# Performance work log

Hardware: AMD Instinct MI355X
Metric: run time of the kernel (lower is better)

## Reference

```python
import jax, jax.numpy as jnp
import numpy as np

N = 50000        # nodes
E_RAND = 800000  # random edges (avg degree 16)
F_IN = 512       # num_features
H = 128          # h_dim * num_heads = 16 * 8
C = 40           # num_classes
NEG_SLOPE = 0.2  # GATv2 default


def _glorot(key, shape):
    lim = float(np.sqrt(6.0 / (shape[0] + shape[1])))
    return jax.random.uniform(key, shape, jnp.float32, -lim, lim)


def setup_inputs() -> dict:
    key = jax.random.key(0)
    ks = jax.random.split(key, 12)
    src = jax.random.randint(ks[0], (E_RAND,), 0, N)
    dst = jax.random.randint(ks[1], (E_RAND,), 0, N)
    loop = jnp.arange(N)  # self-loops (GATv2Conv add_self_loops=True)
    edge_index = jnp.stack([jnp.concatenate([src, loop]),
                            jnp.concatenate([dst, loop])]).astype(jnp.int32)
    x = jax.random.normal(ks[2], (N, F_IN), jnp.float32)
    return {
        "x": x,
        "edge_index": edge_index,
        "W1l": _glorot(ks[3], (F_IN, H)), "b1l": jnp.zeros((H,), jnp.float32),
        "W1r": _glorot(ks[4], (F_IN, H)), "b1r": jnp.zeros((H,), jnp.float32),
        "a1": _glorot(ks[5], (H, 1)).reshape(H),
        "bias1": jnp.zeros((H,), jnp.float32),
        "W2l": _glorot(ks[6], (H, C)), "b2l": jnp.zeros((C,), jnp.float32),
        "W2r": _glorot(ks[7], (H, C)), "b2r": jnp.zeros((C,), jnp.float32),
        "a2": _glorot(ks[8], (C, 1)).reshape(C),
        "bias2": jnp.zeros((C,), jnp.float32),
    }


def gatv2_layer(x, src, dst, Wl, bl, Wr, br, att, bias, n):
    # PyG GATv2Conv, heads=1: xl = lin_l(x) (source side), xr = lin_r(x) (target side)
    xl = x @ Wl + bl                                   # [N, C_out]
    xr = x @ Wr + br                                   # [N, C_out]
    # edge score e_ij = a^T LeakyReLU(xl[j] + xr[i])
    e = jax.nn.leaky_relu(xl[src] + xr[dst], negative_slope=NEG_SLOPE) @ att  # [E]
    # segment softmax over edges grouped by destination node
    m = jax.ops.segment_max(e, dst, num_segments=n)    # every node has a self-loop
    ex = jnp.exp(e - m[dst])
    den = jax.ops.segment_sum(ex, dst, num_segments=n)
    alpha = ex / den[dst]                              # [E]
    # weighted scatter-aggregate of source-transformed features
    out = jax.ops.segment_sum(alpha[:, None] * xl[src], dst, num_segments=n)
    return out + bias


def reference(x, edge_index, W1l, b1l, W1r, b1r, a1, bias1,
              W2l, b2l, W2r, b2r, a2, bias2):
    # eval mode: dropout(p=0.6) is identity
    src, dst = edge_index[0], edge_index[1]
    n = x.shape[0]
    h = gatv2_layer(x, src, dst, W1l, b1l, W1r, b1r, a1, bias1, n)
    h = jax.nn.elu(h)
    h = gatv2_layer(h, src, dst, W2l, b2l, W2r, b2r, a2, bias2, n)
    return (h, jax.nn.log_softmax(h, axis=1))
```

## Files before the change

kernel.cpp:

```cpp
#include <hip/hip_runtime.h>
#include <hip/hip_bf16.h>
#include <math.h>

#define FIN 512
#define H1 128
#define C2 40
#define C2P 64

typedef __attribute__((ext_vector_type(8))) short short8;
typedef __attribute__((ext_vector_type(4))) float f32x4;

__device__ __forceinline__ ushort f2bf(float f) {
    union { float f; unsigned u; } c; c.f = f;
    unsigned u = c.u;
    return (ushort)((u + 0x7fffu + ((u >> 16) & 1u)) >> 16);
}
__device__ __forceinline__ float bf2f_lo(unsigned u) { return __uint_as_float(u << 16); }
__device__ __forceinline__ float bf2f_hi(unsigned u) { return __uint_as_float(u & 0xffff0000u); }

__device__ __forceinline__ short bfc(float f) {
    __hip_bfloat16 h = __float2bfloat16(f);
    return *reinterpret_cast<short*>(&h);
}

__device__ __forceinline__ void gload_lds16(const void* g, void* l) {
    __builtin_amdgcn_global_load_lds(
        (const __attribute__((address_space(1))) void*)g,
        (__attribute__((address_space(3))) void*)l, 16, 0, 0);
}

__global__ void count_k(const int* __restrict__ dst, int* __restrict__ cnt, int E) {
    int e = blockIdx.x * 256 + threadIdx.x;
    if (e < E) atomicAdd(&cnt[dst[e] + 1], 1);
}

__global__ __launch_bounds__(1024) void scan_k(int* __restrict__ arr, int ntot) {
    __shared__ int part[1024];
    int t = threadIdx.x;
    int chunk = (((ntot + 1023) / 1024) + 3) & ~3;
    int b = t * chunk;
    int s = 0;
    bool full = (b + chunk <= ntot);
    if (full) {
#pragma unroll 4
        for (int j = 0; j < chunk; j += 4) {
            int4 v = *reinterpret_cast<const int4*>(&arr[b + j]);
            s += v.x + v.y + v.z + v.w;
        }
    } else {
        for (int j = b; j < ntot; j++) s += arr[j];
    }
    part[t] = s;
    __syncthreads();
    for (int off = 1; off < 1024; off <<= 1) {
        int v = (t >= off) ? part[t - off] : 0;
        __syncthreads();
        part[t] += v;
        __syncthreads();
    }
    int run = (t == 0) ? 0 : part[t - 1];
    if (full) {
        for (int j = 0; j < chunk; j += 4) {
            int4 v = *reinterpret_cast<const int4*>(&arr[b + j]);
            int r0 = run + v.x, r1 = r0 + v.y, r2 = r1 + v.z, r3 = r2 + v.w;
            *reinterpret_cast<int4*>(&arr[b + j]) = make_int4(r0, r1, r2, r3);
            run = r3;
        }
    } else {
        for (int j = b; j < ntot; j++) { run += arr[j]; arr[j] = run; }
    }
}

__global__ void fill_k(const int* __restrict__ src, const int* __restrict__ dst,
                       const int* __restrict__ rowptr, int* __restrict__ fillp,
                       int* __restrict__ csr, int E) {
    int e = blockIdx.x * 256 + threadIdx.x;
    if (e < E) {
        int d = dst[e];
        int p = atomicAdd(&fillp[d], 1);
        csr[rowptr[d] + p] = src[e];
    }
}

__global__ void prep_k(const float* __restrict__ W1l, const float* __restrict__ W1r,
                       ushort* __restrict__ Wt2) {
    int idx = blockIdx.x * 256 + threadIdx.x;
    int kc  = idx >> 11;
    int rem = idx & 2047;
    int col = rem >> 3;
    int j   = rem & 7;
    int k   = kc * 8 + j;
    float v = (col < H1) ? W1l[k * H1 + col] : W1r[k * H1 + (col - H1)];
    Wt2[idx] = f2bf(v);
}

__global__ void prep2_k(const float* __restrict__ W2l, const float* __restrict__ W2r,
                        ushort* __restrict__ Ws) {
    int idx = blockIdx.x * 256 + threadIdx.x;
    if (idx >= 80 * H1) return;
    int col = idx >> 7;
    int k   = idx & 127;
    float v = (col < C2) ? W2l[k * C2 + col] : W2r[k * C2 + (col - C2)];
    Ws[idx] = f2bf(v);
}

__global__ __launch_bounds__(256, 3) void gemm1_k(
    const float* __restrict__ x, const ushort* __restrict__ Wt2,
    const float* __restrict__ bl, const float* __restrict__ br,
    ushort* __restrict__ xlb, float* __restrict__ xr, int n)
{
    __shared__ ushort As[2][64][40];
    __shared__ ushort Bs[2][4 * 256 * 8];

    const int tid  = threadIdx.x;
    const int w    = tid >> 6;
    const int lane = tid & 63;
    const int l15  = lane & 15;
    const int lhi  = lane >> 4;
    const int r0   = blockIdx.x * 64;

    f32x4 acc[4][4];
#pragma unroll
    for (int m = 0; m < 4; m++)
#pragma unroll
        for (int nn = 0; nn < 4; nn++) acc[m][nn] = (f32x4){0.f, 0.f, 0.f, 0.f};

    const int arow = tid >> 2;
    const int akq  = (tid & 3) * 8;
    const int arow_g = min(r0 + arow, n - 1);
    const float* aptr = x + (size_t)arow_g * FIN + akq;

    const char* bsrc = (const char*)Wt2 + (size_t)tid * 16;
    char*       bdst = (char*)Bs + (size_t)tid * 16;

    {
        float4 v0 = *reinterpret_cast<const float4*>(aptr);
        float4 v1 = *reinterpret_cast<const float4*>(aptr + 4);
#pragma unroll
        for (int i = 0; i < 4; i++)
            gload_lds16(bsrc + i * 4096, bdst + i * 4096);
        short8 h0;
        h0[0] = bfc(v0.x); h0[1] = bfc(v0.y); h0[2] = bfc(v0.z); h0[3] = bfc(v0.w);
        h0[4] = bfc(v1.x); h0[5] = bfc(v1.y); h0[6] = bfc(v1.z); h0[7] = bfc(v1.w);
        *reinterpret_cast<short8*>(&As[0][arow][akq]) = h0;
    }
    __syncthreads();

    int cur = 0;
    for (int t = 0; t < 15; ++t) {
        const int nxt = cur ^ 1;

        float4 v0 = *reinterpret_cast<const float4*>(aptr + (t + 1) * 32);
        float4 v1 = *reinterpret_cast<const float4*>(aptr + (t + 1) * 32 + 4);
        {
            const char* bs = bsrc + (size_t)(t + 1) * 16384;
            char*       bd = bdst + (size_t)nxt * 16384;
#pragma unroll
            for (int i = 0; i < 4; i++)
                gload_lds16(bs + i * 4096, bd + i * 4096);
        }

        short8 af[4], bf4[4];
#pragma unroll
        for (int m = 0; m < 4; m++)
            af[m] = *reinterpret_cast<const short8*>(&As[cur][m * 16 + l15][lhi * 8]);
#pragma unroll
        for (int nn = 0; nn < 4; nn++)
            bf4[nn] = *reinterpret_cast<const short8*>(
                &Bs[cur][(lhi * 256 + w * 64 + nn * 16 + l15) * 8]);
#pragma unroll
        for (int m = 0; m < 4; m++)
#pragma unroll
            for (int nn = 0; nn < 4; nn++)
                acc[m][nn] = __builtin_amdgcn_mfma_f32_16x16x32_bf16(af[m], bf4[nn], acc[m][nn], 0, 0, 0);

        short8 h0;
        h0[0] = bfc(v0.x); h0[1] = bfc(v0.y); h0[2] = bfc(v0.z); h0[3] = bfc(v0.w);
        h0[4] = bfc(v1.x); h0[5] = bfc(v1.y); h0[6] = bfc(v1.z); h0[7] = bfc(v1.w);
        *reinterpret_cast<short8*>(&As[nxt][arow][akq]) = h0;

        __syncthreads();
        cur = nxt;
    }

    {
        short8 af[4], bf4[4];
#pragma unroll
        for (int m = 0; m < 4; m++)
            af[m] = *reinterpret_cast<const short8*>(&As[cur][m * 16 + l15][lhi * 8]);
#pragma unroll
        for (int nn = 0; nn < 4; nn++)
            bf4[nn] = *reinterpret_cast<const short8*>(
                &Bs[cur][(lhi * 256 + w * 64 + nn * 16 + l15) * 8]);
#pragma unroll
        for (int m = 0; m < 4; m++)
#pragma unroll
            for (int nn = 0; nn < 4; nn++)
                acc[m][nn] = __builtin_amdgcn_mfma_f32_16x16x32_bf16(af[m], bf4[nn], acc[m][nn], 0, 0, 0);
    }

#pragma unroll
    for (int nn = 0; nn < 4; nn++) {
        int col = w * 64 + nn * 16 + l15;
        bool left = (col < H1);
        float bias = left ? bl[col] : br[col - H1];
#pragma unroll
        for (int m = 0; m < 4; m++) {
#pragma unroll
            for (int r = 0; r < 4; r++) {
                int row = r0 + m * 16 + lhi * 4 + r;
                if (row < n) {
                    float v = acc[m][nn][r] + bias;
                    if (left) xlb[(size_t)row * H1 + col] = f2bf(v);
                    else      xr [(size_t)row * H1 + (col - H1)] = v;
                }
            }
        }
    }
}

__global__ __launch_bounds__(256) void edge1_k(
    const ushort* __restrict__ xlb, const float* xr,
    const int* __restrict__ rowptr, const int* __restrict__ csr,
    const float* __restrict__ att, const float* __restrict__ bias,
    float* h, int n)
{
    int wid  = threadIdx.x >> 6;
    int lane = threadIdx.x & 63;
    int grp  = lane >> 4;
    int gl   = lane & 15;
    int i = blockIdx.x * 4 + wid;
    if (i >= n) return;

    const float* xrp = &xr[(size_t)i * H1 + gl * 8];
    float4 xr0 = *reinterpret_cast<const float4*>(xrp);
    float4 xr1v = *reinterpret_cast<const float4*>(xrp + 4);
    float xrv[8] = {xr0.x, xr0.y, xr0.z, xr0.w, xr1v.x, xr1v.y, xr1v.z, xr1v.w};
    float4 a0 = *reinterpret_cast<const float4*>(&att[gl * 8]);
    float4 a1 = *reinterpret_cast<const float4*>(&att[gl * 8 + 4]);
    float av[8] = {a0.x, a0.y, a0.z, a0.w, a1.x, a1.y, a1.z, a1.w};

    int e0 = rowptr[i], e1 = rowptr[i + 1];

    float m = -INFINITY, den = 0.f;
    float acc[8];
#pragma unroll
    for (int f = 0; f < 8; f++) acc[f] = 0.f;

    int e = e0 + grp;
    uint4 u0, u1;
    if (e < e1) {
        int s = csr[e];
        u0 = *reinterpret_cast<const uint4*>(&xlb[(size_t)s * H1 + gl * 8]);
    }
    if (e + 4 < e1) {
        int s = csr[e + 4];
        u1 = *reinterpret_cast<const uint4*>(&xlb[(size_t)s * H1 + gl * 8]);
    }
    while (e < e1) {
        uint4 cu = u0;
        u0 = u1;
        if (e + 8 < e1) {
            int s2 = csr[e + 8];
            u1 = *reinterpret_cast<const uint4*>(&xlb[(size_t)s2 * H1 + gl * 8]);
        }
        float xlv[8];
        xlv[0] = bf2f_lo(cu.x); xlv[1] = bf2f_hi(cu.x);
        xlv[2] = bf2f_lo(cu.y); xlv[3] = bf2f_hi(cu.y);
        xlv[4] = bf2f_lo(cu.z); xlv[5] = bf2f_hi(cu.z);
        xlv[6] = bf2f_lo(cu.w); xlv[7] = bf2f_hi(cu.w);
        float p = 0.f;
#pragma unroll
        for (int f = 0; f < 8; f++) {
            float t = xlv[f] + xrv[f];
            t = t > 0.f ? t : 0.2f * t;
            p += t * av[f];
        }
#pragma unroll
        for (int o = 8; o > 0; o >>= 1) p += __shfl_xor(p, o);
        float mn = fmaxf(m, p);
        float sc = __expf(m - mn);
        float wgt = __expf(p - mn);
        den = den * sc + wgt;
#pragma unroll
        for (int f = 0; f < 8; f++) acc[f] = acc[f] * sc + wgt * xlv[f];
        m = mn;
        e += 4;
    }

    float mstar = m;
    mstar = fmaxf(mstar, __shfl_xor(mstar, 16));
    mstar = fmaxf(mstar, __shfl_xor(mstar, 32));
    float scale = __expf(m - mstar);
    den *= scale;
#pragma unroll
    for (int f = 0; f < 8; f++) acc[f] *= scale;
    den += __shfl_xor(den, 16); den += __shfl_xor(den, 32);
#pragma unroll
    for (int f = 0; f < 8; f++) {
        acc[f] += __shfl_xor(acc[f], 16);
        acc[f] += __shfl_xor(acc[f], 32);
    }

    if (grp == 0) {
        float inv = 1.f / den;
        float o[8];
#pragma unroll
        for (int f = 0; f < 8; f++) {
            float v = acc[f] * inv + bias[gl * 8 + f];
            o[f] = v > 0.f ? v : expm1f(v);
        }
        float* hp = &h[(size_t)i * H1 + gl * 8];
        *reinterpret_cast<float4*>(hp)     = make_float4(o[0], o[1], o[2], o[3]);
        *reinterpret_cast<float4*>(hp + 4) = make_float4(o[4], o[5], o[6], o[7]);
    }
}

__global__ __launch_bounds__(256) void gemm2_k(
    const float* __restrict__ h, const ushort* __restrict__ Ws,
    const float* __restrict__ bl, const float* __restrict__ br,
    ushort* __restrict__ xl2b, float* __restrict__ xr2, int n)
{
    __shared__ ushort WsL[80][136];

    const int tid = threadIdx.x;
    const int w    = tid >> 6;
    const int lane = tid & 63;
    const int l15  = lane & 15;
    const int lhi  = lane >> 4;
    const int r0 = blockIdx.x * 64;

#pragma unroll
    for (int q = 0; q < 5; q++) {
        int c = tid + q * 256;
        int col = c >> 4;
        int k0  = (c & 15) * 8;
        *reinterpret_cast<short8*>(&WsL[col][k0]) =
            *reinterpret_cast<const short8*>(&Ws[col * H1 + k0]);
    }
    __syncthreads();

    const int arow = min(r0 + w * 16 + l15, n - 1);
    const float* ap = &h[(size_t)arow * H1 + lhi * 8];

    f32x4 acc[5];
#pragma unroll
    for (int nt = 0; nt < 5; nt++) acc[nt] = (f32x4){0.f, 0.f, 0.f, 0.f};

#pragma unroll
    for (int kc = 0; kc < 4; kc++) {
        float4 v0 = *reinterpret_cast<const float4*>(ap + kc * 32);
        float4 v1 = *reinterpret_cast<const float4*>(ap + kc * 32 + 4);
        short8 af;
        af[0] = bfc(v0.x); af[1] = bfc(v0.y);
        af[2] = bfc(v0.z); af[3] = bfc(v0.w);
        af[4] = bfc(v1.x); af[5] = bfc(v1.y);
        af[6] = bfc(v1.z); af[7] = bfc(v1.w);
#pragma unroll
        for (int nt = 0; nt < 5; nt++) {
            short8 bf = *reinterpret_cast<const short8*>(&WsL[nt * 16 + l15][kc * 32 + lhi * 8]);
            acc[nt] = __builtin_amdgcn_mfma_f32_16x16x32_bf16(af, bf, acc[nt], 0, 0, 0);
        }
    }

#pragma unroll
    for (int nt = 0; nt < 5; nt++) {
        int col = nt * 16 + l15;
        float bias = (col < C2) ? bl[col] : br[col - C2];
#pragma unroll
        for (int r = 0; r < 4; r++) {
            int row = r0 + w * 16 + lhi * 4 + r;
            if (row < n) {
                float v = acc[nt][r] + bias;
                if (col < C2) xl2b[(size_t)row * C2P + col] = f2bf(v);
                else          xr2 [(size_t)row * C2  + (col - C2)] = v;
            }
        }
    }
    {
        int row = r0 + w * 16 + l15;
        int part = lhi;
        if (part < 3 && row < n) {
            uint4 z = make_uint4(0u, 0u, 0u, 0u);
            *reinterpret_cast<uint4*>(&xl2b[(size_t)row * C2P + C2 + part * 8]) = z;
        }
    }
}

__global__ __launch_bounds__(256) void edge2_k(
    const ushort* __restrict__ xl2b, const float* __restrict__ xr2,
    const int* __restrict__ rowptr, const int* __restrict__ csr,
    const float* __restrict__ att, const float* __restrict__ bias,
    float* __restrict__ out, int n)
{
    int wid  = threadIdx.x >> 6;
    int lane = threadIdx.x & 63;
    int grp  = lane >> 3;
    int gl   = lane & 7;
    int i = blockIdx.x * 4 + wid;
    if (i >= n) return;

    float xrv[8], av[8];
#pragma unroll
    for (int f = 0; f < 8; f++) {
        int idx = gl * 8 + f;
        bool real = idx < C2;
        xrv[f] = real ? xr2[(size_t)i * C2 + idx] : 0.f;
        av[f]  = real ? att[idx] : 0.f;
    }

    int e0 = rowptr[i], e1 = rowptr[i + 1];

    float m = -INFINITY, den = 0.f;
    float acc[8];
#pragma unroll
    for (int f = 0; f < 8; f++) acc[f] = 0.f;

    int e = e0 + grp;
    uint4 u0, u1;
    if (e < e1) {
        int s = csr[e];
        u0 = *reinterpret_cast<const uint4*>(&xl2b[(size_t)s * C2P + gl * 8]);
    }
    if (e + 8 < e1) {
        int s = csr[e + 8];
        u1 = *reinterpret_cast<const uint4*>(&xl2b[(size_t)s * C2P + gl * 8]);
    }
    while (e < e1) {
        uint4 cu = u0;
        u0 = u1;
        if (e + 16 < e1) {
            int s2 = csr[e + 16];
            u1 = *reinterpret_cast<const uint4*>(&xl2b[(size_t)s2 * C2P + gl * 8]);
        }
        float xlv[8];
        xlv[0] = bf2f_lo(cu.x); xlv[1] = bf2f_hi(cu.x);
        xlv[2] = bf2f_lo(cu.y); xlv[3] = bf2f_hi(cu.y);
        xlv[4] = bf2f_lo(cu.z); xlv[5] = bf2f_hi(cu.z);
        xlv[6] = bf2f_lo(cu.w); xlv[7] = bf2f_hi(cu.w);
        float p = 0.f;
#pragma unroll
        for (int f = 0; f < 8; f++) {
            float t = xlv[f] + xrv[f];
            t = t > 0.f ? t : 0.2f * t;
            p += t * av[f];
        }
#pragma unroll
        for (int o = 4; o > 0; o >>= 1) p += __shfl_xor(p, o);
        float mn = fmaxf(m, p);
        float sc = __expf(m - mn);
        float wgt = __expf(p - mn);
        den = den * sc + wgt;
#pragma unroll
        for (int f = 0; f < 8; f++) acc[f] = acc[f] * sc + wgt * xlv[f];
        m = mn;
        e += 8;
    }

    float mstar = m;
    mstar = fmaxf(mstar, __shfl_xor(mstar, 8));
    mstar = fmaxf(mstar, __shfl_xor(mstar, 16));
    mstar = fmaxf(mstar, __shfl_xor(mstar, 32));
    float scale = __expf(m - mstar);
    den *= scale;
#pragma unroll
    for (int f = 0; f < 8; f++) acc[f] *= scale;
    den += __shfl_xor(den, 8); den += __shfl_xor(den, 16); den += __shfl_xor(den, 32);
#pragma unroll
    for (int f = 0; f < 8; f++) {
        acc[f] += __shfl_xor(acc[f], 8);
        acc[f] += __shfl_xor(acc[f], 16);
        acc[f] += __shfl_xor(acc[f], 32);
    }

    float inv = 1.f / den;
    bool real_lane = gl < 5;
    float o[8];
#pragma unroll
    for (int f = 0; f < 8; f++) {
        int idx = gl * 8 + f;
        o[f] = acc[f] * inv + (idx < C2 ? bias[idx] : 0.f);
    }

    float mv = -INFINITY;
    if (real_lane) {
#pragma unroll
        for (int f = 0; f < 8; f++) mv = fmaxf(mv, o[f]);
    }
    mv = fmaxf(mv, __shfl_xor(mv, 1));
    mv = fmaxf(mv, __shfl_xor(mv, 2));
    mv = fmaxf(mv, __shfl_xor(mv, 4));
    float se = 0.f;
    if (real_lane) {
#pragma unroll
        for (int f = 0; f < 8; f++) se += __expf(o[f] - mv);
    }
    se += __shfl_xor(se, 1); se += __shfl_xor(se, 2); se += __shfl_xor(se, 4);
    float lse = mv + logf(se);

    if (grp == 0 && real_lane) {
        float* op = &out[(size_t)i * C2 + gl * 8];
        *reinterpret_cast<float4*>(op)     = make_float4(o[0], o[1], o[2], o[3]);
        *reinterpret_cast<float4*>(op + 4) = make_float4(o[4], o[5], o[6], o[7]);
        float* lp = &out[(size_t)n * C2 + (size_t)i * C2 + gl * 8];
        *reinterpret_cast<float4*>(lp)     = make_float4(o[0] - lse, o[1] - lse, o[2] - lse, o[3] - lse);
        *reinterpret_cast<float4*>(lp + 4) = make_float4(o[4] - lse, o[5] - lse, o[6] - lse, o[7] - lse);
    }
}

extern "C" void kernel_launch(void* const* d_in, const int* in_sizes, int n_in,
                              void* d_out, int out_size, void* d_ws, size_t ws_size,
                              hipStream_t stream) {
    const float* x    = (const float*)d_in[0];
    const int*   ei   = (const int*)  d_in[1];
    const float* W1l  = (const float*)d_in[2];
    const float* b1l  = (const float*)d_in[3];
    const float* W1r  = (const float*)d_in[4];
    const float* b1r  = (const float*)d_in[5];
    const float* a1   = (const float*)d_in[6];
    const float* bias1= (const float*)d_in[7];
    const float* W2l  = (const float*)d_in[8];
    const float* b2l  = (const float*)d_in[9];
    const float* W2r  = (const float*)d_in[10];
    const float* b2r  = (const float*)d_in[11];
    const float* a2   = (const float*)d_in[12];
    const float* bias2= (const float*)d_in[13];

    const int N = in_sizes[0] / FIN;
    const int E = in_sizes[1] / 2;
    const int* src = ei;
    const int* dst = ei + E;

    float*  xr1 = (float*)d_ws;
    float*  xr2 = xr1 + (size_t)N * H1;
    ushort* xlb = (ushort*)(xr2 + (size_t)N * C2);
    ushort* xl2b = xlb;
    ushort* Wt2 = xlb + (size_t)N * H1;
    ushort* Ws2 = Wt2 + 131072;
    int* rowptr = (int*)(Ws2 + 10240);
    int* fillp  = rowptr + (N + 1);
    int* csr    = fillp + N;

    hipMemsetAsync(rowptr, 0, sizeof(int) * (size_t)(2 * N + 1), stream);
    count_k<<<(E + 255) / 256, 256, 0, stream>>>(dst, rowptr, E);
    scan_k<<<1, 1024, 0, stream>>>(rowptr, N + 1);
    fill_k<<<(E + 255) / 256, 256, 0, stream>>>(src, dst, rowptr, fillp, csr, E);

    prep_k<<<512, 256, 0, stream>>>(W1l, W1r, Wt2);
    prep2_k<<<40, 256, 0, stream>>>(W2l, W2r, Ws2);
    gemm1_k<<<(N + 63) / 64, 256, 0, stream>>>(x, Wt2, b1l, b1r, xlb, xr1, N);
    edge1_k<<<(N + 3) / 4, 256, 0, stream>>>(xlb, xr1, rowptr, csr, a1, bias1, xr1, N);
    gemm2_k<<<(N + 63) / 64, 256, 0, stream>>>(xr1, Ws2, b2l, b2r, xl2b, xr2, N);
    edge2_k<<<(N + 3) / 4, 256, 0, stream>>>(xl2b, xr2, rowptr, csr, a2, bias2, (float*)d_out, N);
}
```

Measured before the change: 306.3 us.

## Split gemm1 output columns across two blocks and merge prep kernels into count

Merges the edge-count, W1 prep and W2 prep kernels into one launch to cut launch overhead. Splits gemm1 so each block computes either the xl or the xr half (128 columns), doubling the grid, halving the B tile and accumulator registers, and raising the occupancy hint to 6. The trade-off is that every x tile is now read and converted to bf16 twice, once per half, in exchange for more parallelism and occupancy.

```diff
diff --git a/kernel.cpp b/kernel.cpp
--- a/kernel.cpp
+++ b/kernel.cpp
@@ -29,9 +29,34 @@
         (__attribute__((address_space(3))) void*)l, 16, 0, 0);
 }
 
-__global__ void count_k(const int* __restrict__ dst, int* __restrict__ cnt, int E) {
-    int e = blockIdx.x * 256 + threadIdx.x;
-    if (e < E) atomicAdd(&cnt[dst[e] + 1], 1);
+__global__ void aux_k(const int* __restrict__ dst, int* __restrict__ cnt, int E, int EB,
+                      const float* __restrict__ W1l, const float* __restrict__ W1r,
+                      ushort* __restrict__ Wt2,
+                      const float* __restrict__ W2l, const float* __restrict__ W2r,
+                      ushort* __restrict__ Ws) {
+    int b = blockIdx.x;
+    int t = threadIdx.x;
+    if (b < EB) {
+        int e = b * 256 + t;
+        if (e < E) atomicAdd(&cnt[dst[e] + 1], 1);
+    } else if (b < EB + 512) {
+        int idx = (b - EB) * 256 + t;
+        int kc  = idx >> 11;
+        int rem = idx & 2047;
+        int col = rem >> 3;
+        int j   = rem & 7;
+        int k   = kc * 8 + j;
+        float v = (col < H1) ? W1l[k * H1 + col] : W1r[k * H1 + (col - H1)];
+        Wt2[idx] = f2bf(v);
+    } else {
+        int idx = (b - EB - 512) * 256 + t;
+        if (idx < 80 * H1) {
+            int col = idx >> 7;
+            int k   = idx & 127;
+            float v = (col < C2) ? W2l[k * C2 + col] : W2r[k * C2 + (col - C2)];
+            Ws[idx] = f2bf(v);
+        }
+    }
 }
 
 __global__ __launch_bounds__(1024) void scan_k(int* __restrict__ arr, int ntot) {
@@ -82,63 +107,44 @@
     }
 }
 
-__global__ void prep_k(const float* __restrict__ W1l, const float* __restrict__ W1r,
-                       ushort* __restrict__ Wt2) {
-    int idx = blockIdx.x * 256 + threadIdx.x;
-    int kc  = idx >> 11;
-    int rem = idx & 2047;
-    int col = rem >> 3;
-    int j   = rem & 7;
-    int k   = kc * 8 + j;
-    float v = (col < H1) ? W1l[k * H1 + col] : W1r[k * H1 + (col - H1)];
-    Wt2[idx] = f2bf(v);
-}
-
-__global__ void prep2_k(const float* __restrict__ W2l, const float* __restrict__ W2r,
-                        ushort* __restrict__ Ws) {
-    int idx = blockIdx.x * 256 + threadIdx.x;
-    if (idx >= 80 * H1) return;
-    int col = idx >> 7;
-    int k   = idx & 127;
-    float v = (col < C2) ? W2l[k * C2 + col] : W2r[k * C2 + (col - C2)];
-    Ws[idx] = f2bf(v);
-}
-
-__global__ __launch_bounds__(256, 3) void gemm1_k(
+__global__ __launch_bounds__(256, 6) void gemm1_k(
     const float* __restrict__ x, const ushort* __restrict__ Wt2,
     const float* __restrict__ bl, const float* __restrict__ br,
     ushort* __restrict__ xlb, float* __restrict__ xr, int n)
 {
     __shared__ ushort As[2][64][40];
-    __shared__ ushort Bs[2][4 * 256 * 8];
+    __shared__ ushort Bs[2][4 * 128 * 8];
 
     const int tid  = threadIdx.x;
     const int w    = tid >> 6;
     const int lane = tid & 63;
     const int l15  = lane & 15;
     const int lhi  = lane >> 4;
-    const int r0   = blockIdx.x * 64;
-
-    f32x4 acc[4][4];
+    const int bm   = blockIdx.x >> 1;
+    const int half = blockIdx.x & 1;
+    const int r0   = bm * 64;
+    const int c0   = half * 128;
+
+    f32x4 acc[4][2];
 #pragma unroll
     for (int m = 0; m < 4; m++)
 #pragma unroll
-        for (int nn = 0; nn < 4; nn++) acc[m][nn] = (f32x4){0.f, 0.f, 0.f, 0.f};
+        for (int nn = 0; nn < 2; nn++) acc[m][nn] = (f32x4){0.f, 0.f, 0.f, 0.f};
 
     const int arow = tid >> 2;
     const int akq  = (tid & 3) * 8;
     const int arow_g = min(r0 + arow, n - 1);
     const float* aptr = x + (size_t)arow_g * FIN + akq;
 
-    const char* bsrc = (const char*)Wt2 + (size_t)tid * 16;
-    char*       bdst = (char*)Bs + (size_t)tid * 16;
+    const char* bsrc = (const char*)Wt2 + ((size_t)w * 256 + c0) * 16 + (size_t)lane * 16;
+    char*       bdst = (char*)Bs + (size_t)w * 2048 + (size_t)lane * 16;
 
     {
+#pragma unroll
+        for (int h2 = 0; h2 < 2; h2++)
+            gload_lds16(bsrc + h2 * 1024, bdst + h2 * 1024);
         float4 v0 = *reinterpret_cast<const float4*>(aptr);
         float4 v1 = *reinterpret_cast<const float4*>(aptr + 4);
-#pragma unroll
-        for (int i = 0; i < 4; i++)
-            gload_lds16(bsrc + i * 4096, bdst + i * 4096);
         short8 h0;
         h0[0] = bfc(v0.x); h0[1] = bfc(v0.y); h0[2] = bfc(v0.z); h0[3] = bfc(v0.w);
         h0[4] = bfc(v1.x); h0[5] = bfc(v1.y); h0[6] = bfc(v1.z); h0[7] = bfc(v1.w);
@@ -154,25 +160,25 @@
         float4 v1 = *reinterpret_cast<const float4*>(aptr + (t + 1) * 32 + 4);
         {
             const char* bs = bsrc + (size_t)(t + 1) * 16384;
-            char*       bd = bdst + (size_t)nxt * 16384;
-#pragma unroll
-            for (int i = 0; i < 4; i++)
-                gload_lds16(bs + i * 4096, bd + i * 4096);
-        }
-
-        short8 af[4], bf4[4];
+            char*       bd = bdst + (size_t)nxt * 8192;
+#pragma unroll
+            for (int h2 = 0; h2 < 2; h2++)
+                gload_lds16(bs + h2 * 1024, bd + h2 * 1024);
+        }
+
+        short8 af[4], bf2[2];
 #pragma unroll
         for (int m = 0; m < 4; m++)
             af[m] = *reinterpret_cast<const short8*>(&As[cur][m * 16 + l15][lhi * 8]);
 #pragma unroll
-        for (int nn = 0; nn < 4; nn++)
-            bf4[nn] = *reinterpret_cast<const short8*>(
-                &Bs[cur][(lhi * 256 + w * 64 + nn * 16 + l15) * 8]);
+        for (int nn = 0; nn < 2; nn++)
+            bf2[nn] = *reinterpret_cast<const short8*>(
+                &Bs[cur][(lhi * 128 + w * 32 + nn * 16 + l15) * 8]);
 #pragma unroll
         for (int m = 0; m < 4; m++)
 #pragma unroll
-            for (int nn = 0; nn < 4; nn++)
-                acc[m][nn] = __builtin_amdgcn_mfma_f32_16x16x32_bf16(af[m], bf4[nn], acc[m][nn], 0, 0, 0);
+            for (int nn = 0; nn < 2; nn++)
+                acc[m][nn] = __builtin_amdgcn_mfma_f32_16x16x32_bf16(af[m], bf2[nn], acc[m][nn], 0, 0, 0);
 
         short8 h0;
         h0[0] = bfc(v0.x); h0[1] = bfc(v0.y); h0[2] = bfc(v0.z); h0[3] = bfc(v0.w);
@@ -184,26 +190,25 @@
     }
 
     {
-        short8 af[4], bf4[4];
+        short8 af[4], bf2[2];
 #pragma unroll
         for (int m = 0; m < 4; m++)
             af[m] = *reinterpret_cast<const short8*>(&As[cur][m * 16 + l15][lhi * 8]);
 #pragma unroll
-        for (int nn = 0; nn < 4; nn++)
-            bf4[nn] = *reinterpret_cast<const short8*>(
-                &Bs[cur][(lhi * 256 + w * 64 + nn * 16 + l15) * 8]);
+        for (int nn = 0; nn < 2; nn++)
+            bf2[nn] = *reinterpret_cast<const short8*>(
+                &Bs[cur][(lhi * 128 + w * 32 + nn * 16 + l15) * 8]);
 #pragma unroll
         for (int m = 0; m < 4; m++)
 #pragma unroll
-            for (int nn = 0; nn < 4; nn++)
-                acc[m][nn] = __builtin_amdgcn_mfma_f32_16x16x32_bf16(af[m], bf4[nn], acc[m][nn], 0, 0, 0);
-    }
-
-#pragma unroll
-    for (int nn = 0; nn < 4; nn++) {
-        int col = w * 64 + nn * 16 + l15;
-        bool left = (col < H1);
-        float bias = left ? bl[col] : br[col - H1];
+            for (int nn = 0; nn < 2; nn++)
+                acc[m][nn] = __builtin_amdgcn_mfma_f32_16x16x32_bf16(af[m], bf2[nn], acc[m][nn], 0, 0, 0);
+    }
+
+#pragma unroll
+    for (int nn = 0; nn < 2; nn++) {
+        int col = w * 32 + nn * 16 + l15;
+        float bias = half ? br[col] : bl[col];
 #pragma unroll
         for (int m = 0; m < 4; m++) {
 #pragma unroll
@@ -211,8 +216,8 @@
                 int row = r0 + m * 16 + lhi * 4 + r;
                 if (row < n) {
                     float v = acc[m][nn][r] + bias;
-                    if (left) xlb[(size_t)row * H1 + col] = f2bf(v);
-                    else      xr [(size_t)row * H1 + (col - H1)] = v;
+                    if (half) xr [(size_t)row * H1 + col] = v;
+                    else      xlb[(size_t)row * H1 + col] = f2bf(v);
                 }
             }
         }
@@ -541,14 +546,14 @@
     int* fillp  = rowptr + (N + 1);
     int* csr    = fillp + N;
 
+    const int EB = (E + 255) / 256;
+
     hipMemsetAsync(rowptr, 0, sizeof(int) * (size_t)(2 * N + 1), stream);
-    count_k<<<(E + 255) / 256, 256, 0, stream>>>(dst, rowptr, E);
+    aux_k<<<EB + 552, 256, 0, stream>>>(dst, rowptr, E, EB, W1l, W1r, Wt2, W2l, W2r, Ws2);
     scan_k<<<1, 1024, 0, stream>>>(rowptr, N + 1);
-    fill_k<<<(E + 255) / 256, 256, 0, stream>>>(src, dst, rowptr, fillp, csr, E);
-
-    prep_k<<<512, 256, 0, stream>>>(W1l, W1r, Wt2);
-    prep2_k<<<40, 256, 0, stream>>>(W2l, W2r, Ws2);
-    gemm1_k<<<(N + 63) / 64, 256, 0, stream>>>(x, Wt2, b1l, b1r, xlb, xr1, N);
+    fill_k<<<EB, 256, 0, stream>>>(src, dst, rowptr, fillp, csr, E);
+
+    gemm1_k<<<((N + 63) / 64) * 2, 256, 0, stream>>>(x, Wt2, b1l, b1r, xlb, xr1, N);
     edge1_k<<<(N + 3) / 4, 256, 0, stream>>>(xlb, xr1, rowptr, csr, a1, bias1, xr1, N);
     gemm2_k<<<(N + 63) / 64, 256, 0, stream>>>(xr1, Ws2, b2l, b2r, xl2b, xr2, N);
     edge2_k<<<(N + 3) / 4, 256, 0, stream>>>(xl2b, xr2, rowptr, csr, a2, bias2, (float*)d_out, N);
```

New measurement: 302.1 us. Within noise of the previous version (-1.4%).

## Stage full A tile in LDS, stream B from global via registers; merge prep kernels

Applied to the files above, without the earlier changes.

The first GEMM now loads the entire 64x512 row block of x into LDS as bf16 once, instead of double-buffering 32-wide K slices with a barrier per step. B fragments are read directly from global (L2-resident weights) into registers, with two register sets alternating as a prefetch. Occupancy drops from 3 to 2 blocks per CU because the LDS tile is larger. Separately, the edge-count, W1 and W2 prep kernels are fused into one launch to cut launch overhead.

```diff
diff --git a/kernel.cpp b/kernel.cpp
--- a/kernel.cpp
+++ b/kernel.cpp
@@ -23,15 +23,34 @@
     return *reinterpret_cast<short*>(&h);
 }
 
-__device__ __forceinline__ void gload_lds16(const void* g, void* l) {
-    __builtin_amdgcn_global_load_lds(
-        (const __attribute__((address_space(1))) void*)g,
-        (__attribute__((address_space(3))) void*)l, 16, 0, 0);
-}
-
-__global__ void count_k(const int* __restrict__ dst, int* __restrict__ cnt, int E) {
-    int e = blockIdx.x * 256 + threadIdx.x;
-    if (e < E) atomicAdd(&cnt[dst[e] + 1], 1);
+__global__ void aux_k(const int* __restrict__ dst, int* __restrict__ cnt, int E, int EB,
+                      const float* __restrict__ W1l, const float* __restrict__ W1r,
+                      ushort* __restrict__ Wt2,
+                      const float* __restrict__ W2l, const float* __restrict__ W2r,
+                      ushort* __restrict__ Ws) {
+    int b = blockIdx.x;
+    int t = threadIdx.x;
+    if (b < EB) {
+        int e = b * 256 + t;
+        if (e < E) atomicAdd(&cnt[dst[e] + 1], 1);
+    } else if (b < EB + 512) {
+        int idx = (b - EB) * 256 + t;
+        int kc  = idx >> 11;
+        int rem = idx & 2047;
+        int col = rem >> 3;
+        int j   = rem & 7;
+        int k   = kc * 8 + j;
+        float v = (col < H1) ? W1l[k * H1 + col] : W1r[k * H1 + (col - H1)];
+        Wt2[idx] = f2bf(v);
+    } else {
+        int idx = (b - EB - 512) * 256 + t;
+        if (idx < 80 * H1) {
+            int col = idx >> 7;
+            int k   = idx & 127;
+            float v = (col < C2) ? W2l[k * C2 + col] : W2r[k * C2 + (col - C2)];
+            Ws[idx] = f2bf(v);
+        }
+    }
 }
 
 __global__ __launch_bounds__(1024) void scan_k(int* __restrict__ arr, int ntot) {
@@ -82,35 +101,12 @@
     }
 }
 
-__global__ void prep_k(const float* __restrict__ W1l, const float* __restrict__ W1r,
-                       ushort* __restrict__ Wt2) {
-    int idx = blockIdx.x * 256 + threadIdx.x;
-    int kc  = idx >> 11;
-    int rem = idx & 2047;
-    int col = rem >> 3;
-    int j   = rem & 7;
-    int k   = kc * 8 + j;
-    float v = (col < H1) ? W1l[k * H1 + col] : W1r[k * H1 + (col - H1)];
-    Wt2[idx] = f2bf(v);
-}
-
-__global__ void prep2_k(const float* __restrict__ W2l, const float* __restrict__ W2r,
-                        ushort* __restrict__ Ws) {
-    int idx = blockIdx.x * 256 + threadIdx.x;
-    if (idx >= 80 * H1) return;
-    int col = idx >> 7;
-    int k   = idx & 127;
-    float v = (col < C2) ? W2l[k * C2 + col] : W2r[k * C2 + (col - C2)];
-    Ws[idx] = f2bf(v);
-}
-
-__global__ __launch_bounds__(256, 3) void gemm1_k(
+__global__ __launch_bounds__(256, 2) void gemm1_k(
     const float* __restrict__ x, const ushort* __restrict__ Wt2,
     const float* __restrict__ bl, const float* __restrict__ br,
     ushort* __restrict__ xlb, float* __restrict__ xr, int n)
 {
-    __shared__ ushort As[2][64][40];
-    __shared__ ushort Bs[2][4 * 256 * 8];
+    __shared__ ushort As[64][552];
 
     const int tid  = threadIdx.x;
     const int w    = tid >> 6;
@@ -119,84 +115,73 @@
     const int lhi  = lane >> 4;
     const int r0   = blockIdx.x * 64;
 
+    const ushort* bp = Wt2 + ((size_t)(w * 64 + l15)) * 8;
+
+    short8 bfA[4], bfB[4];
+#pragma unroll
+    for (int nn = 0; nn < 4; nn++)
+        bfA[nn] = *reinterpret_cast<const short8*>(bp + (0 * 4 + lhi) * 2048 + nn * 128);
+#pragma unroll
+    for (int nn = 0; nn < 4; nn++)
+        bfB[nn] = *reinterpret_cast<const short8*>(bp + (1 * 4 + lhi) * 2048 + nn * 128);
+
+    {
+        const int srow = tid >> 2;
+        const int skc  = (tid & 3) * 128;
+        const int srow_g = min(r0 + srow, n - 1);
+        const float* sp = x + (size_t)srow_g * FIN + skc;
+#pragma unroll
+        for (int j = 0; j < 16; j++) {
+            float4 a = *reinterpret_cast<const float4*>(sp + j * 8);
+            float4 b = *reinterpret_cast<const float4*>(sp + j * 8 + 4);
+            short8 h;
+            h[0] = bfc(a.x); h[1] = bfc(a.y); h[2] = bfc(a.z); h[3] = bfc(a.w);
+            h[4] = bfc(b.x); h[5] = bfc(b.y); h[6] = bfc(b.z); h[7] = bfc(b.w);
+            *reinterpret_cast<short8*>(&As[srow][skc + j * 8]) = h;
+        }
+    }
+    __syncthreads();
+
     f32x4 acc[4][4];
 #pragma unroll
     for (int m = 0; m < 4; m++)
 #pragma unroll
         for (int nn = 0; nn < 4; nn++) acc[m][nn] = (f32x4){0.f, 0.f, 0.f, 0.f};
 
-    const int arow = tid >> 2;
-    const int akq  = (tid & 3) * 8;
-    const int arow_g = min(r0 + arow, n - 1);
-    const float* aptr = x + (size_t)arow_g * FIN + akq;
-
-    const char* bsrc = (const char*)Wt2 + (size_t)tid * 16;
-    char*       bdst = (char*)Bs + (size_t)tid * 16;
-
-    {
-        float4 v0 = *reinterpret_cast<const float4*>(aptr);
-        float4 v1 = *reinterpret_cast<const float4*>(aptr + 4);
-#pragma unroll
-        for (int i = 0; i < 4; i++)
-            gload_lds16(bsrc + i * 4096, bdst + i * 4096);
-        short8 h0;
-        h0[0] = bfc(v0.x); h0[1] = bfc(v0.y); h0[2] = bfc(v0.z); h0[3] = bfc(v0.w);
-        h0[4] = bfc(v1.x); h0[5] = bfc(v1.y); h0[6] = bfc(v1.z); h0[7] = bfc(v1.w);
-        *reinterpret_cast<short8*>(&As[0][arow][akq]) = h0;
-    }
-    __syncthreads();
-
-    int cur = 0;
-    for (int t = 0; t < 15; ++t) {
-        const int nxt = cur ^ 1;
-
-        float4 v0 = *reinterpret_cast<const float4*>(aptr + (t + 1) * 32);
-        float4 v1 = *reinterpret_cast<const float4*>(aptr + (t + 1) * 32 + 4);
+#pragma unroll
+    for (int ks = 0; ks < 16; ks += 2) {
         {
-            const char* bs = bsrc + (size_t)(t + 1) * 16384;
-            char*       bd = bdst + (size_t)nxt * 16384;
-#pragma unroll
-            for (int i = 0; i < 4; i++)
-                gload_lds16(bs + i * 4096, bd + i * 4096);
-        }
-
-        short8 af[4], bf4[4];
-#pragma unroll
-        for (int m = 0; m < 4; m++)
-            af[m] = *reinterpret_cast<const short8*>(&As[cur][m * 16 + l15][lhi * 8]);
-#pragma unroll
-        for (int nn = 0; nn < 4; nn++)
-            bf4[nn] = *reinterpret_cast<const short8*>(
-                &Bs[cur][(lhi * 256 + w * 64 + nn * 16 + l15) * 8]);
-#pragma unroll
-        for (int m = 0; m < 4; m++)
-#pragma unroll
-            for (int nn = 0; nn < 4; nn++)
-                acc[m][nn] = __builtin_amdgcn_mfma_f32_16x16x32_bf16(af[m], bf4[nn], acc[m][nn], 0, 0, 0);
-
-        short8 h0;
-        h0[0] = bfc(v0.x); h0[1] = bfc(v0.y); h0[2] = bfc(v0.z); h0[3] = bfc(v0.w);
-        h0[4] = bfc(v1.x); h0[5] = bfc(v1.y); h0[6] = bfc(v1.z); h0[7] = bfc(v1.w);
-        *reinterpret_cast<short8*>(&As[nxt][arow][akq]) = h0;
-
-        __syncthreads();
-        cur = nxt;
-    }
-
-    {
-        short8 af[4], bf4[4];
-#pragma unroll
-        for (int m = 0; m < 4; m++)
-            af[m] = *reinterpret_cast<const short8*>(&As[cur][m * 16 + l15][lhi * 8]);
-#pragma unroll
-        for (int nn = 0; nn < 4; nn++)
-            bf4[nn] = *reinterpret_cast<const short8*>(
-                &Bs[cur][(lhi * 256 + w * 64 + nn * 16 + l15) * 8]);
-#pragma unroll
-        for (int m = 0; m < 4; m++)
-#pragma unroll
-            for (int nn = 0; nn < 4; nn++)
-                acc[m][nn] = __builtin_amdgcn_mfma_f32_16x16x32_bf16(af[m], bf4[nn], acc[m][nn], 0, 0, 0);
+            short8 af[4];
+#pragma unroll
+            for (int m = 0; m < 4; m++)
+                af[m] = *reinterpret_cast<const short8*>(&As[m * 16 + l15][ks * 32 + lhi * 8]);
+#pragma unroll
+            for (int m = 0; m < 4; m++)
+#pragma unroll
+                for (int nn = 0; nn < 4; nn++)
+                    acc[m][nn] = __builtin_amdgcn_mfma_f32_16x16x32_bf16(af[m], bfA[nn], acc[m][nn], 0, 0, 0);
+            if (ks + 2 < 16) {
+#pragma unroll
+                for (int nn = 0; nn < 4; nn++)
+                    bfA[nn] = *reinterpret_cast<const short8*>(bp + ((ks + 2) * 4 + lhi) * 2048 + nn * 128);
+            }
+        }
+        {
+            short8 af[4];
+#pragma unroll
+            for (int m = 0; m < 4; m++)
+                af[m] = *reinterpret_cast<const short8*>(&As[m * 16 + l15][(ks + 1) * 32 + lhi * 8]);
+#pragma unroll
+            for (int m = 0; m < 4; m++)
+#pragma unroll
+                for (int nn = 0; nn < 4; nn++)
+                    acc[m][nn] = __builtin_amdgcn_mfma_f32_16x16x32_bf16(af[m], bfB[nn], acc[m][nn], 0, 0, 0);
+            if (ks + 3 < 16) {
+#pragma unroll
+                for (int nn = 0; nn < 4; nn++)
+                    bfB[nn] = *reinterpret_cast<const short8*>(bp + ((ks + 3) * 4 + lhi) * 2048 + nn * 128);
+            }
+        }
     }
 
 #pragma unroll
@@ -541,13 +526,13 @@
     int* fillp  = rowptr + (N + 1);
     int* csr    = fillp + N;
 
+    const int EB = (E + 255) / 256;
+
     hipMemsetAsync(rowptr, 0, sizeof(int) * (size_t)(2 * N + 1), stream);
-    count_k<<<(E + 255) / 256, 256, 0, stream>>>(dst, rowptr, E);
+    aux_k<<<EB + 552, 256, 0, stream>>>(dst, rowptr, E, EB, W1l, W1r, Wt2, W2l, W2r, Ws2);
     scan_k<<<1, 1024, 0, stream>>>(rowptr, N + 1);
-    fill_k<<<(E + 255) / 256, 256, 0, stream>>>(src, dst, rowptr, fillp, csr, E);
-
-    prep_k<<<512, 256, 0, stream>>>(W1l, W1r, Wt2);
-    prep2_k<<<40, 256, 0, stream>>>(W2l, W2r, Ws2);
+    fill_k<<<EB, 256, 0, stream>>>(src, dst, rowptr, fillp, csr, E);
+
     gemm1_k<<<(N + 63) / 64, 256, 0, stream>>>(x, Wt2, b1l, b1r, xlb, xr1, N);
     edge1_k<<<(N + 3) / 4, 256, 0, stream>>>(xlb, xr1, rowptr, csr, a1, bias1, xr1, N);
     gemm2_k<<<(N + 63) / 64, 256, 0, stream>>>(xr1, Ws2, b2l, b2r, xl2b, xr2, N);
```

Measured after the change: 306.8 us. No clear change (+0.2%).
